# Performance work log

Hardware: AMD Instinct MI355X
Metric: run time of the kernel (lower is better)

Reference implementation:

```python
import jax, jax.numpy as jnp
import numpy as np

K = 4096          # num_embeddings
D = 64            # embedding_dim
BETA = 0.25       # commitment_cost
DECAY = 0.99      # EMA decay
EPS = 1e-5        # Laplace smoothing eps


def setup_inputs() -> dict:
    key = jax.random.key(0)
    k1, k2, k3 = jax.random.split(key, 3)
    inputs = jax.random.normal(k1, (32, 1024, D), dtype=jnp.float32)
    weight = jax.random.normal(k2, (K, D), dtype=jnp.float32) * (1.0 / K)
    ema_cluster_size = jnp.ones((K,), dtype=jnp.float32)
    ema_embedding_sum = jax.random.normal(k3, (K, D), dtype=jnp.float32) * (1.0 / K)
    return {
        "inputs": inputs,
        "weight": weight,
        "ema_cluster_size": ema_cluster_size,
        "ema_embedding_sum": ema_embedding_sum,
    }


def reference(inputs, weight, ema_cluster_size, ema_embedding_sum):
    input_shape = inputs.shape
    flat = inputs.reshape(-1, D)                       # (N, D)
    distances = (
        jnp.sum(flat * flat, axis=1, keepdims=True)
        + jnp.sum(weight * weight, axis=1)
        - 2.0 * (flat @ weight.T)
    )
    encoding_indices = jnp.argmin(distances, axis=1)   # (N,) int
    quantized = weight[encoding_indices].reshape(input_shape)

    # EMA codebook update (torch does this with a one-hot (N,K) matmul;
    # segment_sum is the same math without the dense intermediate)
    new_cluster_size = jax.ops.segment_sum(
        jnp.ones_like(encoding_indices, dtype=jnp.float32), encoding_indices,
        num_segments=K)
    new_embedding_sum = jax.ops.segment_sum(flat, encoding_indices,
                                            num_segments=K)
    ema_cs = DECAY * ema_cluster_size + (1.0 - DECAY) * new_cluster_size
    ema_es = DECAY * ema_embedding_sum + (1.0 - DECAY) * new_embedding_sum
    n = jnp.sum(ema_cs)
    cs_smoothed = (ema_cs + EPS) / (n + K * EPS) * n
    new_weight = ema_es / cs_smoothed[:, None]

    # Commitment loss: beta * mse(inputs, sg(quantized))
    commitment_loss = BETA * jnp.mean(
        (inputs - jax.lax.stop_gradient(quantized)) ** 2)
    # Straight-through estimator
    quantized_st = inputs + jax.lax.stop_gradient(quantized - inputs)

    return (quantized_st, commitment_loss, encoding_indices,
            new_weight, ema_cs, ema_es)
```

## Files before the change

### kernel.cpp

```cpp
#include <hip/hip_runtime.h>

#define N_VEC   32768
#define K_CODES 4096
#define D_DIM   64
#define NELEM   2097152
#define TH_APPROX 7.5e-4f

#define OUT0_OFF 0
#define OUT1_OFF 2097152
#define OUT2_OFF 2097153
#define OUT3_OFF 2129921
#define OUT4_OFF 2392065
#define OUT5_OFF 2396161

#define WS_BNORM   0
#define WS_COUNTS  16384
#define WS_CANDC   32768
#define WS_CANDS   163840
#define WS_SUMS    163840
#define WS_WBF     1212416
#define WS_LPART   1212416
#define WS_CSPART  1277952

typedef short  s16x8 __attribute__((ext_vector_type(8)));
typedef float  f32x4 __attribute__((ext_vector_type(4)));

__device__ __forceinline__ unsigned short bf16rne(float f) {
    unsigned u = __float_as_uint(f);
    unsigned r = u + 0x7fffu + ((u >> 16) & 1u);
    return (unsigned short)(r >> 16);
}

__device__ __forceinline__ float np_pairwise64(const float* sq) {
    float r0 = sq[0], r1 = sq[1], r2 = sq[2], r3 = sq[3];
    float r4 = sq[4], r5 = sq[5], r6 = sq[6], r7 = sq[7];
#pragma unroll
    for (int b = 8; b < 64; b += 8) {
        r0 = __fadd_rn(r0, sq[b + 0]); r1 = __fadd_rn(r1, sq[b + 1]);
        r2 = __fadd_rn(r2, sq[b + 2]); r3 = __fadd_rn(r3, sq[b + 3]);
        r4 = __fadd_rn(r4, sq[b + 4]); r5 = __fadd_rn(r5, sq[b + 5]);
        r6 = __fadd_rn(r6, sq[b + 6]); r7 = __fadd_rn(r7, sq[b + 7]);
    }
    return __fadd_rn(__fadd_rn(__fadd_rn(r0, r1), __fadd_rn(r2, r3)),
                     __fadd_rn(__fadd_rn(r4, r5), __fadd_rn(r6, r7)));
}

__global__ void k_bnorm(const float* __restrict__ w, float* __restrict__ bn) {
    int k = blockIdx.x * 256 + threadIdx.x;
    const float* wr = w + k * D_DIM;
    float sq[64];
#pragma unroll
    for (int i = 0; i < 64; ++i) { float v = wr[i]; sq[i] = __fmul_rn(v, v); }
    bn[k] = np_pairwise64(sq);
}

__global__ void k_wcvtbf(const float* __restrict__ w, short* __restrict__ wbf) {
    int gid = blockIdx.x * 256 + threadIdx.x;
    wbf[gid] = (short)bf16rne(w[gid]);
}

#define XLDS_LD 72

__global__ __launch_bounds__(256, 2) void k_approx(
    const float* __restrict__ x, const short* __restrict__ wbf,
    const float* __restrict__ bn, int* __restrict__ candc,
    unsigned short* __restrict__ cands) {
    __shared__ short xlds[64 * XLDS_LD];
    __shared__ float wmin[4][64];
    __shared__ float gmin[64];
    __shared__ int   ccnt[64];

    const int tid  = threadIdx.x;
    const int lane = tid & 63;
    const int wid  = __builtin_amdgcn_readfirstlane(tid >> 6);
    const int rbase = blockIdx.x * 64;
    const int arow = lane & 15;
    const int agrp = lane >> 4;

    for (int i = tid; i < 64 * 16; i += 256) {
        int r = i >> 4, c4 = i & 15;
        float4 v = ((const float4*)(x + (size_t)(rbase + r) * D_DIM))[c4];
        ushort4 b;
        b.x = bf16rne(v.x); b.y = bf16rne(v.y);
        b.z = bf16rne(v.z); b.w = bf16rne(v.w);
        *(ushort4*)&xlds[r * XLDS_LD + c4 * 4] = b;
    }
    if (tid < 64) ccnt[tid] = 0;
    __syncthreads();

    s16x8 af0[4], af1[4];
#pragma unroll
    for (int rt = 0; rt < 4; ++rt) {
        af0[rt] = *(const s16x8*)&xlds[(rt * 16 + arow) * XLDS_LD + 0 * 32 + agrp * 8];
        af1[rt] = *(const s16x8*)&xlds[(rt * 16 + arow) * XLDS_LD + 1 * 32 + agrp * 8];
    }

    const int col0base = wid * 1024;

    float rm[16];
#pragma unroll
    for (int i = 0; i < 16; ++i) rm[i] = 3.4e38f;

    for (int tc = 0; tc < 64; ++tc) {
        const int mycol = col0base + tc * 16 + arow;
        s16x8 b0 = *(const s16x8*)&wbf[(size_t)mycol * D_DIM + 0 * 32 + agrp * 8];
        s16x8 b1 = *(const s16x8*)&wbf[(size_t)mycol * D_DIM + 1 * 32 + agrp * 8];
        float bnv = bn[mycol];
#pragma unroll
        for (int rt = 0; rt < 4; ++rt) {
            f32x4 c = {0.f, 0.f, 0.f, 0.f};
            c = __builtin_amdgcn_mfma_f32_16x16x32_bf16(af0[rt], b0, c, 0, 0, 0);
            c = __builtin_amdgcn_mfma_f32_16x16x32_bf16(af1[rt], b1, c, 0, 0, 0);
#pragma unroll
            for (int j = 0; j < 4; ++j) {
                float m = fmaf(-2.0f, c[j], bnv);
                rm[rt * 4 + j] = fminf(rm[rt * 4 + j], m);
            }
        }
    }

#pragma unroll
    for (int i = 0; i < 16; ++i) {
        float v = rm[i];
        v = fminf(v, __shfl_xor(v, 1));
        v = fminf(v, __shfl_xor(v, 2));
        v = fminf(v, __shfl_xor(v, 4));
        v = fminf(v, __shfl_xor(v, 8));
        rm[i] = v;
    }
    if (arow == 0) {
#pragma unroll
        for (int i = 0; i < 16; ++i)
            wmin[wid][(i >> 2) * 16 + agrp * 4 + (i & 3)] = rm[i];
    }
    __syncthreads();
    if (tid < 64) {
        float g = fminf(fminf(wmin[0][tid], wmin[1][tid]),
                        fminf(wmin[2][tid], wmin[3][tid]));
        gmin[tid] = g + TH_APPROX;
    }
    __syncthreads();

    float gv[16];
#pragma unroll
    for (int i = 0; i < 16; ++i)
        gv[i] = gmin[(i >> 2) * 16 + agrp * 4 + (i & 3)];

    for (int tc = 0; tc < 64; ++tc) {
        const int mycol = col0base + tc * 16 + arow;
        s16x8 b0 = *(const s16x8*)&wbf[(size_t)mycol * D_DIM + 0 * 32 + agrp * 8];
        s16x8 b1 = *(const s16x8*)&wbf[(size_t)mycol * D_DIM + 1 * 32 + agrp * 8];
        float bnv = bn[mycol];
#pragma unroll
        for (int rt = 0; rt < 4; ++rt) {
            f32x4 c = {0.f, 0.f, 0.f, 0.f};
            c = __builtin_amdgcn_mfma_f32_16x16x32_bf16(af0[rt], b0, c, 0, 0, 0);
            c = __builtin_amdgcn_mfma_f32_16x16x32_bf16(af1[rt], b1, c, 0, 0, 0);
#pragma unroll
            for (int j = 0; j < 4; ++j) {
                float m = fmaf(-2.0f, c[j], bnv);
                if (m <= gv[rt * 4 + j]) {
                    int row = rt * 16 + agrp * 4 + j;
                    int p = atomicAdd(&ccnt[row], 1);
                    if (p < 16)
                        cands[(size_t)(rbase + row) * 16 + p] = (unsigned short)mycol;
                }
            }
        }
    }
    __syncthreads();
    if (tid < 64) candc[rbase + tid] = ccnt[tid];
}

__global__ __launch_bounds__(256) void k_rescore(
    const float* __restrict__ x, const float* __restrict__ w,
    const float* __restrict__ bn, const int* __restrict__ candc,
    const unsigned short* __restrict__ cands, float* __restrict__ out_idx) {
    const int n = blockIdx.x * 256 + threadIdx.x;

    float4 xv[16];
    const float4* xr = (const float4*)(x + (size_t)n * D_DIM);
#pragma unroll
    for (int i = 0; i < 16; ++i) xv[i] = xr[i];

    float A;
    {
        float sq[64];
#pragma unroll
        for (int i = 0; i < 16; ++i) {
            sq[4*i+0] = __fmul_rn(xv[i].x, xv[i].x);
            sq[4*i+1] = __fmul_rn(xv[i].y, xv[i].y);
            sq[4*i+2] = __fmul_rn(xv[i].z, xv[i].z);
            sq[4*i+3] = __fmul_rn(xv[i].w, xv[i].w);
        }
        A = np_pairwise64(sq);
    }

    const int cnt = candc[n];
    float bestd = 3.4e38f;
    int   besti = 0;

    if (cnt <= 16) {
        unsigned short cl[16];
        for (int i = 0; i < cnt; ++i) cl[i] = cands[(size_t)n * 16 + i];
        for (int i = 1; i < cnt; ++i) {
            unsigned short v = cl[i];
            int j = i - 1;
            while (j >= 0 && cl[j] > v) { cl[j + 1] = cl[j]; --j; }
            cl[j + 1] = v;
        }
        for (int i = 0; i < cnt; ++i) {
            const int c = cl[i];
            const float4* wr = (const float4*)(w + (size_t)c * D_DIM);
            float a = 0.f;
#pragma unroll
            for (int ch = 0; ch < 16; ++ch) {
                float4 u = wr[ch];
                a = __fmaf_rn(xv[ch].x, u.x, a);
                a = __fmaf_rn(xv[ch].y, u.y, a);
                a = __fmaf_rn(xv[ch].z, u.z, a);
                a = __fmaf_rn(xv[ch].w, u.w, a);
            }
            float d = __fsub_rn(__fadd_rn(A, bn[c]), __fmul_rn(2.0f, a));
            if (d < bestd) { bestd = d; besti = c; }
        }
    } else {
        for (int c = 0; c < K_CODES; ++c) {
            const float4* wr = (const float4*)(w + (size_t)c * D_DIM);
            float a = 0.f;
#pragma unroll
            for (int ch = 0; ch < 16; ++ch) {
                float4 u = wr[ch];
                a = __fmaf_rn(xv[ch].x, u.x, a);
                a = __fmaf_rn(xv[ch].y, u.y, a);
                a = __fmaf_rn(xv[ch].z, u.z, a);
                a = __fmaf_rn(xv[ch].w, u.w, a);
            }
            float d = __fsub_rn(__fadd_rn(A, bn[c]), __fmul_rn(2.0f, a));
            if (d < bestd) { bestd = d; besti = c; }
        }
    }
    out_idx[n] = (float)besti;
}

__global__ __launch_bounds__(256) void k_quant(
    const float* __restrict__ x, const float* __restrict__ w,
    const float* __restrict__ idxf, float* __restrict__ out0,
    float* __restrict__ sums, int* __restrict__ counts,
    double* __restrict__ lpart) {
    const int gid = blockIdx.x * 256 + threadIdx.x;
    const int n = gid >> 6, d = gid & 63;
    const int idx = (int)idxf[n];
    const float in = x[gid];
    const float q  = w[idx * D_DIM + d];
    out0[gid] = in + (q - in);
    const float diff = in - q;
    atomicAdd(&sums[idx * D_DIM + d], in);
    if (d == 0) atomicAdd(&counts[idx], 1);

    __shared__ double red[256];
    red[threadIdx.x] = (double)diff * (double)diff;
    __syncthreads();
    for (int s = 128; s > 0; s >>= 1) {
        if (threadIdx.x < s) red[threadIdx.x] += red[threadIdx.x + s];
        __syncthreads();
    }
    if (threadIdx.x == 0) lpart[blockIdx.x] = red[0];
}

__global__ void k_loss(const double* __restrict__ lpart, float* __restrict__ out1) {
    __shared__ double red[256];
    double s = 0.0;
    for (int i = threadIdx.x; i < 8192; i += 256) s += lpart[i];
    red[threadIdx.x] = s;
    __syncthreads();
    for (int st = 128; st > 0; st >>= 1) {
        if (threadIdx.x < st) red[threadIdx.x] += red[threadIdx.x + st];
        __syncthreads();
    }
    if (threadIdx.x == 0) out1[0] = (float)(0.25 * red[0] / (double)NELEM);
}

__global__ void k_emacs(const float* __restrict__ old_cs, const int* __restrict__ counts,
                        float* __restrict__ out4, double* __restrict__ cspart) {
    const int k = blockIdx.x * 256 + threadIdx.x;
    const float e = 0.99f * old_cs[k] + 0.01f * (float)counts[k];
    out4[k] = e;
    __shared__ double red[256];
    red[threadIdx.x] = (double)e;
    __syncthreads();
    for (int s = 128; s > 0; s >>= 1) {
        if (threadIdx.x < s) red[threadIdx.x] += red[threadIdx.x + s];
        __syncthreads();
    }
    if (threadIdx.x == 0) cspart[blockIdx.x] = red[0];
}

__global__ __launch_bounds__(256) void k_final(
    const float* __restrict__ old_es, const float* __restrict__ sums,
    const float* __restrict__ out4, const double* __restrict__ cspart,
    float* __restrict__ out3, float* __restrict__ out5) {
    double nd = 0.0;
#pragma unroll
    for (int i = 0; i < 16; ++i) nd += cspart[i];
    const float nf = (float)nd;
    const int gid = blockIdx.x * 256 + threadIdx.x;
    const int k = gid >> 6;
    const float es = 0.99f * old_es[gid] + 0.01f * sums[gid];
    out5[gid] = es;
    const float cs = out4[k];
    const float cssm = (cs + 1e-5f) / (nf + 4096.0f * 1e-5f) * nf;
    out3[gid] = es / cssm;
}

extern "C" void kernel_launch(void* const* d_in, const int* in_sizes, int n_in,
                              void* d_out, int out_size, void* d_ws, size_t ws_size,
                              hipStream_t stream) {
    const float* x      = (const float*)d_in[0];
    const float* w      = (const float*)d_in[1];
    const float* old_cs = (const float*)d_in[2];
    const float* old_es = (const float*)d_in[3];

    float* o    = (float*)d_out;
    float* out0 = o + OUT0_OFF;
    float* out1 = o + OUT1_OFF;
    float* out2 = o + OUT2_OFF;
    float* out3 = o + OUT3_OFF;
    float* out4 = o + OUT4_OFF;
    float* out5 = o + OUT5_OFF;

    char* ws = (char*)d_ws;
    float*          bnorm  = (float*)(ws + WS_BNORM);
    int*            counts = (int*)(ws + WS_COUNTS);
    int*            candc  = (int*)(ws + WS_CANDC);
    unsigned short* cands  = (unsigned short*)(ws + WS_CANDS);
    float*          sums   = (float*)(ws + WS_SUMS);
    short*          wbf    = (short*)(ws + WS_WBF);
    double*         lpart  = (double*)(ws + WS_LPART);
    double*         cspart = (double*)(ws + WS_CSPART);

    hipMemsetAsync(counts, 0, K_CODES * sizeof(int), stream);

    k_bnorm<<<K_CODES / 256, 256, 0, stream>>>(w, bnorm);
    k_wcvtbf<<<K_CODES * D_DIM / 256, 256, 0, stream>>>(w, wbf);
    k_approx<<<N_VEC / 64, 256, 0, stream>>>(x, wbf, bnorm, candc, cands);
    k_rescore<<<N_VEC / 256, 256, 0, stream>>>(x, w, bnorm, candc, cands, out2);
    hipMemsetAsync(sums, 0, K_CODES * D_DIM * sizeof(float), stream);
    k_quant<<<NELEM / 256, 256, 0, stream>>>(x, w, out2, out0, sums, counts, lpart);
    k_loss<<<1, 256, 0, stream>>>(lpart, out1);
    k_emacs<<<K_CODES / 256, 256, 0, stream>>>(old_cs, counts, out4, cspart);
    k_final<<<K_CODES * D_DIM / 256, 256, 0, stream>>>(old_es, sums, out4, cspart,
                                                       out3, out5);
}
```

Baseline: 167.9 us.

## Split approximate argmin into two codebook-chunked kernels for more parallelism

```diff
diff --git a/kernel.cpp b/kernel.cpp
--- a/kernel.cpp
+++ b/kernel.cpp
@@ -21,6 +21,7 @@
 #define WS_WBF     1212416
 #define WS_LPART   1212416
 #define WS_CSPART  1277952
+#define WS_PMIN    1736704
 
 typedef short  s16x8 __attribute__((ext_vector_type(8)));
 typedef float  f32x4 __attribute__((ext_vector_type(4)));
@@ -61,50 +62,53 @@
 
 #define XLDS_LD 72
 
-__global__ __launch_bounds__(256, 2) void k_approx(
+#define STAGE_X_BF16                                                        \
+    for (int i = tid; i < 64 * 16; i += 256) {                              \
+        int r = i >> 4, c4 = i & 15;                                        \
+        float4 v = ((const float4*)(x + (size_t)(rbase + r) * D_DIM))[c4];  \
+        ushort4 b;                                                          \
+        b.x = bf16rne(v.x); b.y = bf16rne(v.y);                             \
+        b.z = bf16rne(v.z); b.w = bf16rne(v.w);                             \
+        *(ushort4*)&xlds[r * XLDS_LD + c4 * 4] = b;                         \
+    }
+
+#define HOIST_A_FRAGS                                                       \
+    s16x8 af0[4], af1[4];                                                   \
+    _Pragma("unroll")                                                       \
+    for (int rt = 0; rt < 4; ++rt) {                                        \
+        af0[rt] = *(const s16x8*)&xlds[(rt * 16 + arow) * XLDS_LD + agrp * 8]; \
+        af1[rt] = *(const s16x8*)&xlds[(rt * 16 + arow) * XLDS_LD + 32 + agrp * 8]; \
+    }
+
+__global__ __launch_bounds__(256, 4) void k_min(
     const float* __restrict__ x, const short* __restrict__ wbf,
-    const float* __restrict__ bn, int* __restrict__ candc,
-    unsigned short* __restrict__ cands) {
+    const float* __restrict__ bn, float* __restrict__ pmin) {
     __shared__ short xlds[64 * XLDS_LD];
     __shared__ float wmin[4][64];
-    __shared__ float gmin[64];
-    __shared__ int   ccnt[64];
 
     const int tid  = threadIdx.x;
     const int lane = tid & 63;
     const int wid  = __builtin_amdgcn_readfirstlane(tid >> 6);
-    const int rbase = blockIdx.x * 64;
+    const int rg   = blockIdx.x & 511;
+    const int kc   = blockIdx.x >> 9;
+    const int rbase = rg * 64;
     const int arow = lane & 15;
     const int agrp = lane >> 4;
 
-    for (int i = tid; i < 64 * 16; i += 256) {
-        int r = i >> 4, c4 = i & 15;
-        float4 v = ((const float4*)(x + (size_t)(rbase + r) * D_DIM))[c4];
-        ushort4 b;
-        b.x = bf16rne(v.x); b.y = bf16rne(v.y);
-        b.z = bf16rne(v.z); b.w = bf16rne(v.w);
-        *(ushort4*)&xlds[r * XLDS_LD + c4 * 4] = b;
-    }
-    if (tid < 64) ccnt[tid] = 0;
-    __syncthreads();
-
-    s16x8 af0[4], af1[4];
-#pragma unroll
-    for (int rt = 0; rt < 4; ++rt) {
-        af0[rt] = *(const s16x8*)&xlds[(rt * 16 + arow) * XLDS_LD + 0 * 32 + agrp * 8];
-        af1[rt] = *(const s16x8*)&xlds[(rt * 16 + arow) * XLDS_LD + 1 * 32 + agrp * 8];
-    }
-
-    const int col0base = wid * 1024;
+    STAGE_X_BF16
+    __syncthreads();
+    HOIST_A_FRAGS
+
+    const int col0 = kc * 1024 + wid * 256;
 
     float rm[16];
 #pragma unroll
     for (int i = 0; i < 16; ++i) rm[i] = 3.4e38f;
 
-    for (int tc = 0; tc < 64; ++tc) {
-        const int mycol = col0base + tc * 16 + arow;
-        s16x8 b0 = *(const s16x8*)&wbf[(size_t)mycol * D_DIM + 0 * 32 + agrp * 8];
-        s16x8 b1 = *(const s16x8*)&wbf[(size_t)mycol * D_DIM + 1 * 32 + agrp * 8];
+    for (int tc = 0; tc < 16; ++tc) {
+        const int mycol = col0 + tc * 16 + arow;
+        s16x8 b0 = *(const s16x8*)&wbf[(size_t)mycol * D_DIM + agrp * 8];
+        s16x8 b1 = *(const s16x8*)&wbf[(size_t)mycol * D_DIM + 32 + agrp * 8];
         float bnv = bn[mycol];
 #pragma unroll
         for (int rt = 0; rt < 4; ++rt) {
@@ -137,19 +141,47 @@
     if (tid < 64) {
         float g = fminf(fminf(wmin[0][tid], wmin[1][tid]),
                         fminf(wmin[2][tid], wmin[3][tid]));
+        pmin[kc * N_VEC + rbase + tid] = g;
+    }
+}
+
+__global__ __launch_bounds__(256, 4) void k_collect(
+    const float* __restrict__ x, const short* __restrict__ wbf,
+    const float* __restrict__ bn, const float* __restrict__ pmin,
+    int* __restrict__ candc, unsigned short* __restrict__ cands) {
+    __shared__ short xlds[64 * XLDS_LD];
+    __shared__ float gmin[64];
+
+    const int tid  = threadIdx.x;
+    const int lane = tid & 63;
+    const int wid  = __builtin_amdgcn_readfirstlane(tid >> 6);
+    const int rg   = blockIdx.x & 511;
+    const int kc   = blockIdx.x >> 9;
+    const int rbase = rg * 64;
+    const int arow = lane & 15;
+    const int agrp = lane >> 4;
+
+    STAGE_X_BF16
+    if (tid < 64) {
+        const int n = rbase + tid;
+        float g = fminf(fminf(pmin[n], pmin[N_VEC + n]),
+                        fminf(pmin[2 * N_VEC + n], pmin[3 * N_VEC + n]));
         gmin[tid] = g + TH_APPROX;
     }
     __syncthreads();
+    HOIST_A_FRAGS
 
     float gv[16];
 #pragma unroll
     for (int i = 0; i < 16; ++i)
         gv[i] = gmin[(i >> 2) * 16 + agrp * 4 + (i & 3)];
 
-    for (int tc = 0; tc < 64; ++tc) {
-        const int mycol = col0base + tc * 16 + arow;
-        s16x8 b0 = *(const s16x8*)&wbf[(size_t)mycol * D_DIM + 0 * 32 + agrp * 8];
-        s16x8 b1 = *(const s16x8*)&wbf[(size_t)mycol * D_DIM + 1 * 32 + agrp * 8];
+    const int col0 = kc * 1024 + wid * 256;
+
+    for (int tc = 0; tc < 16; ++tc) {
+        const int mycol = col0 + tc * 16 + arow;
+        s16x8 b0 = *(const s16x8*)&wbf[(size_t)mycol * D_DIM + agrp * 8];
+        s16x8 b1 = *(const s16x8*)&wbf[(size_t)mycol * D_DIM + 32 + agrp * 8];
         float bnv = bn[mycol];
 #pragma unroll
         for (int rt = 0; rt < 4; ++rt) {
@@ -160,16 +192,14 @@
             for (int j = 0; j < 4; ++j) {
                 float m = fmaf(-2.0f, c[j], bnv);
                 if (m <= gv[rt * 4 + j]) {
-                    int row = rt * 16 + agrp * 4 + j;
-                    int p = atomicAdd(&ccnt[row], 1);
+                    int n = rbase + rt * 16 + agrp * 4 + j;
+                    int p = atomicAdd(&candc[n], 1);
                     if (p < 16)
-                        cands[(size_t)(rbase + row) * 16 + p] = (unsigned short)mycol;
+                        cands[(size_t)n * 16 + p] = (unsigned short)mycol;
                 }
             }
         }
     }
-    __syncthreads();
-    if (tid < 64) candc[rbase + tid] = ccnt[tid];
 }
 
 __global__ __launch_bounds__(256) void k_rescore(
@@ -338,12 +368,15 @@
     short*          wbf    = (short*)(ws + WS_WBF);
     double*         lpart  = (double*)(ws + WS_LPART);
     double*         cspart = (double*)(ws + WS_CSPART);
+    float*          pmin   = (float*)(ws + WS_PMIN);
 
     hipMemsetAsync(counts, 0, K_CODES * sizeof(int), stream);
+    hipMemsetAsync(candc, 0, N_VEC * sizeof(int), stream);
 
     k_bnorm<<<K_CODES / 256, 256, 0, stream>>>(w, bnorm);
     k_wcvtbf<<<K_CODES * D_DIM / 256, 256, 0, stream>>>(w, wbf);
-    k_approx<<<N_VEC / 64, 256, 0, stream>>>(x, wbf, bnorm, candc, cands);
+    k_min<<<2048, 256, 0, stream>>>(x, wbf, bnorm, pmin);
+    k_collect<<<2048, 256, 0, stream>>>(x, wbf, bnorm, pmin, candc, cands);
     k_rescore<<<N_VEC / 256, 256, 0, stream>>>(x, w, bnorm, candc, cands, out2);
     hipMemsetAsync(sums, 0, K_CODES * D_DIM * sizeof(float), stream);
     k_quant<<<NELEM / 256, 256, 0, stream>>>(x, w, out2, out0, sums, counts, lpart);
```

Result: no change. 166.8 us (-0.7%).
